# Performance work log

Hardware: AMD Instinct MI355X
Metric: run time of the kernel (lower is better)

## Reference

```python
import jax, jax.numpy as jnp
import numpy as np

B, S, E = 16, 4096, 2048
WIN = 64

def setup_inputs() -> dict:
    key = jax.random.key(0)
    k1, k2, k3, k4 = jax.random.split(key, 4)
    x = jax.random.normal(k1, (B, S, E), dtype=jnp.float32)
    mask = jax.random.bernoulli(k2, 0.9, (B, S))  # bool mask, mostly valid tokens
    W = jax.random.normal(k3, (E,), dtype=jnp.float32) / np.sqrt(E)
    b = jax.random.normal(k4, (1,), dtype=jnp.float32)
    return {"x": x, "mask": mask, "W": W, "b": b, "window_size": WIN}

def reference(x, mask, W, b, window_size):
    # linear(embed_dim -> 1) then squeeze(-1): [B, S]
    s = jnp.einsum('bse,e->bs', x, W) + b[0]
    # masked_fill(~mask, 0)
    s = jnp.where(mask, s, jnp.zeros((), dtype=s.dtype))
    # sliding-window mean via cumulative sums (equivalent to unfold(1, W, 1).mean(2))
    cs = jnp.cumsum(s, axis=1)
    cs = jnp.pad(cs, ((0, 0), (1, 0)))  # prepend zero: cs[:, i] = sum of first i elems
    window_means = (cs[:, window_size:] - cs[:, :-window_size]) / window_size  # [B, S-W+1]
    # max over window positions -> [B]
    return window_means.max(axis=1)
```

## Files before the change

### kernel.cpp

```cpp
#include <hip/hip_runtime.h>
#include <math.h>

#define EDIM 2048
#define SLEN 4096

__global__ __launch_bounds__(256) void score_kernel(
    const float* __restrict__ x,
    const int*   __restrict__ mask,
    const float* __restrict__ W,
    const float* __restrict__ bias,
    float* __restrict__ s_out)
{
    __shared__ float4 wsh[EDIM / 4];

    const int tid = threadIdx.x;

    const float4* W4 = (const float4*)W;
    wsh[tid]       = W4[tid];
    wsh[tid + 256] = W4[tid + 256];
    __syncthreads();

    const int wave = tid >> 6;
    const int lane = tid & 63;
    const int row  = blockIdx.x * 4 + wave;

    const float4* x4 = (const float4*)(x + (size_t)row * EDIM);

    float acc = 0.0f;
#pragma unroll
    for (int k = 0; k < 8; ++k) {
        float4 xv = x4[lane + 64 * k];
        float4 wv = wsh[lane + 64 * k];
        acc = fmaf(xv.x, wv.x, acc);
        acc = fmaf(xv.y, wv.y, acc);
        acc = fmaf(xv.z, wv.z, acc);
        acc = fmaf(xv.w, wv.w, acc);
    }

#pragma unroll
    for (int off = 32; off > 0; off >>= 1)
        acc += __shfl_down(acc, off, 64);

    if (lane == 0) {
        float v = mask[row] ? (acc + bias[0]) : 0.0f;
        s_out[row] = v;
    }
}

__global__ __launch_bounds__(256) void window_max_kernel(
    const float* __restrict__ s,
    const int*   __restrict__ win_ptr,
    float* __restrict__ out)
{
    __shared__ float sh[SLEN];
    __shared__ float red[256];

    const int b   = blockIdx.x;
    const int tid = threadIdx.x;
    const float* sb = s + (size_t)b * SLEN;

    for (int i = tid; i < SLEN; i += 256)
        sh[i] = sb[i];
    __syncthreads();

    const int win  = *win_ptr;
    const int npos = SLEN - win + 1;

    float best = -INFINITY;
    for (int p = tid; p < npos; p += 256) {
        float sum = 0.0f;
        for (int j = 0; j < win; ++j)
            sum += sh[p + j];
        best = fmaxf(best, sum);
    }

    red[tid] = best;
    __syncthreads();
    for (int k = 128; k > 0; k >>= 1) {
        if (tid < k) red[tid] = fmaxf(red[tid], red[tid + k]);
        __syncthreads();
    }
    if (tid == 0)
        out[b] = red[0] / (float)win;
}

extern "C" void kernel_launch(void* const* d_in, const int* in_sizes, int n_in,
                              void* d_out, int out_size, void* d_ws, size_t ws_size,
                              hipStream_t stream) {
    const float* x    = (const float*)d_in[0];
    const int*   mask = (const int*)  d_in[1];
    const float* W    = (const float*)d_in[2];
    const float* bias = (const float*)d_in[3];
    const int*   win  = (const int*)  d_in[4];

    float* out = (float*)d_out;
    float* s   = (float*)d_ws;

    const int rows = in_sizes[1];
    const int B    = out_size;

    score_kernel<<<rows / 4, 256, 0, stream>>>(x, mask, W, bias, s);
    window_max_kernel<<<B, 256, 0, stream>>>(s, win, out);
}
```

Before: 686.3 us.

## Process 8 rows per wave in score kernel and use running-sum window scan

```diff
diff --git a/kernel.cpp b/kernel.cpp
--- a/kernel.cpp
+++ b/kernel.cpp
@@ -3,6 +3,9 @@
 
 #define EDIM 2048
 #define SLEN 4096
+#define NROWS (16 * 4096)
+#define SBLOCKS 2048
+#define ROWS_PER_WAVE 8
 
 __global__ __launch_bounds__(256) void score_kernel(
     const float* __restrict__ x,
@@ -14,36 +17,49 @@
     __shared__ float4 wsh[EDIM / 4];
 
     const int tid = threadIdx.x;
-
     const float4* W4 = (const float4*)W;
     wsh[tid]       = W4[tid];
     wsh[tid + 256] = W4[tid + 256];
     __syncthreads();
 
-    const int wave = tid >> 6;
-    const int lane = tid & 63;
-    const int row  = blockIdx.x * 4 + wave;
-
-    const float4* x4 = (const float4*)(x + (size_t)row * EDIM);
-
-    float acc = 0.0f;
-#pragma unroll
-    for (int k = 0; k < 8; ++k) {
-        float4 xv = x4[lane + 64 * k];
-        float4 wv = wsh[lane + 64 * k];
-        acc = fmaf(xv.x, wv.x, acc);
-        acc = fmaf(xv.y, wv.y, acc);
-        acc = fmaf(xv.z, wv.z, acc);
-        acc = fmaf(xv.w, wv.w, acc);
-    }
+    const int lane  = tid & 63;
+    const int gwave = blockIdx.x * 4 + (tid >> 6);
+    const int base  = gwave * ROWS_PER_WAVE;
+    const float b0  = bias[0];
 
 #pragma unroll
-    for (int off = 32; off > 0; off >>= 1)
-        acc += __shfl_down(acc, off, 64);
+    for (int i = 0; i < ROWS_PER_WAVE / 2; ++i) {
+        const int r0 = base + 2 * i;
+        const int r1 = r0 + 1;
+        const float4* x0 = (const float4*)(x + (size_t)r0 * EDIM);
+        const float4* x1 = (const float4*)(x + (size_t)r1 * EDIM);
 
-    if (lane == 0) {
-        float v = mask[row] ? (acc + bias[0]) : 0.0f;
-        s_out[row] = v;
+        float a0 = 0.0f, a1 = 0.0f;
+#pragma unroll
+        for (int k = 0; k < 8; ++k) {
+            float4 v0 = x0[lane + 64 * k];
+            float4 v1 = x1[lane + 64 * k];
+            float4 wv = wsh[lane + 64 * k];
+            a0 = fmaf(v0.x, wv.x, a0);
+            a0 = fmaf(v0.y, wv.y, a0);
+            a0 = fmaf(v0.z, wv.z, a0);
+            a0 = fmaf(v0.w, wv.w, a0);
+            a1 = fmaf(v1.x, wv.x, a1);
+            a1 = fmaf(v1.y, wv.y, a1);
+            a1 = fmaf(v1.z, wv.z, a1);
+            a1 = fmaf(v1.w, wv.w, a1);
+        }
+
+#pragma unroll
+        for (int off = 32; off > 0; off >>= 1) {
+            a0 += __shfl_down(a0, off, 64);
+            a1 += __shfl_down(a1, off, 64);
+        }
+
+        if (lane == 0) {
+            s_out[r0] = mask[r0] ? (a0 + b0) : 0.0f;
+            s_out[r1] = mask[r1] ? (a1 + b0) : 0.0f;
+        }
     }
 }
 
@@ -65,13 +81,27 @@
 
     const int win  = *win_ptr;
     const int npos = SLEN - win + 1;
+    const int per  = (npos + 255) / 256;
+
+    int p0 = tid * per;
+    int p1 = p0 + per;
+    if (p1 > npos) p1 = npos;
 
     float best = -INFINITY;
-    for (int p = tid; p < npos; p += 256) {
+    if (p0 < npos) {
+        const int start = tid & (win - 1) & 63;
         float sum = 0.0f;
-        for (int j = 0; j < win; ++j)
-            sum += sh[p + j];
-        best = fmaxf(best, sum);
+        int off = (start < win) ? start : 0;
+        for (int j = 0; j < win; ++j) {
+            sum += sh[p0 + off];
+            ++off;
+            if (off >= win) off = 0;
+        }
+        best = sum;
+        for (int p = p0 + 1; p < p1; ++p) {
+            sum += sh[p - 1 + win] - sh[p - 1];
+            best = fmaxf(best, sum);
+        }
     }
 
     red[tid] = best;
@@ -96,9 +126,8 @@
     float* out = (float*)d_out;
     float* s   = (float*)d_ws;
 
-    const int rows = in_sizes[1];
-    const int B    = out_size;
+    const int B = out_size;
 
-    score_kernel<<<rows / 4, 256, 0, stream>>>(x, mask, W, bias, s);
+    score_kernel<<<SBLOCKS, 256, 0, stream>>>(x, mask, W, bias, s);
     window_max_kernel<<<B, 256, 0, stream>>>(s, win, out);
 }
```

Result: no change. 694.9 us (+1.3%).
